# Kernel tuning notes

Measured on AMD Instinct MI355X. Metric: run time of the kernel, lower is better.

Reference implementation:

```python
import jax, jax.numpy as jnp
import numpy as np

N_QUBITS = 8          # == hidden_dim
DIM = 2 ** N_QUBITS   # statevector size
EMBED = 512
VOCAB = 50257
SEQ = 128
BATCH = 256


def _cnot_chain_perm(n):
    # CNOT(w,w+1) for w in 0..n-2, then CNOT(n-1,0); wire 0 = MSB.
    f = np.arange(2 ** n)
    pairs = [(w, w + 1) for w in range(n - 1)] + [(n - 1, 0)]
    for c, t in pairs:
        cbit = (f >> (n - 1 - c)) & 1
        f = f ^ (cbit << (n - 1 - t))
    inv = np.empty_like(f)
    inv[f] = np.arange(2 ** n)
    return inv

_PERM_INV = jnp.asarray(_cnot_chain_perm(N_QUBITS))
# signs[j, k] = <j|Z_k|j> = 1 - 2*bit_k(j), wire 0 = MSB
_j = np.arange(DIM)[:, None]
_SIGNS = jnp.asarray(1.0 - 2.0 * ((_j >> (N_QUBITS - 1 - np.arange(N_QUBITS))) & 1), dtype=jnp.float32)


def qlayer(y, theta):
    """RX(y_i) encoder + trainable RX(theta_i) (same axis -> RX(y+theta)),
    CNOT ring, PauliZ expectation per wire.  y: (B, n) -> (B, n)."""
    half = 0.5 * (y + theta)
    c = jnp.cos(half).astype(jnp.complex64)
    s = (-1j) * jnp.sin(half).astype(jnp.complex64)
    B = y.shape[0]
    state = jnp.ones((B, 1), jnp.complex64)
    for w in range(N_QUBITS):  # fixed small structural loop (kron build)
        amp = jnp.stack([c[:, w], s[:, w]], axis=1)  # (B, 2)
        state = (state[:, :, None] * amp[:, None, :]).reshape(B, -1)
    state = state[:, _PERM_INV]                       # apply CNOT ring
    probs = jnp.real(state * jnp.conj(state))         # (B, 2^n)
    return probs @ _SIGNS                             # (B, n)


def setup_inputs() -> dict:
    key = jax.random.key(0)
    ks = jax.random.split(key, 16)
    d_in = EMBED + N_QUBITS
    inp = {
        "sentence": jax.random.randint(ks[0], (SEQ, BATCH), 0, VOCAB),
        "features": jax.random.normal(ks[1], (BATCH, N_QUBITS), jnp.float32),
        "emb_table": 0.02 * jax.random.normal(ks[2], (VOCAB, EMBED), jnp.float32),
        "W_f": 0.05 * jax.random.normal(ks[3], (N_QUBITS, d_in), jnp.float32),
        "b_f": jnp.zeros((N_QUBITS,), jnp.float32),
        "W_i": 0.05 * jax.random.normal(ks[4], (N_QUBITS, d_in), jnp.float32),
        "b_i": jnp.zeros((N_QUBITS,), jnp.float32),
        "W_u": 0.05 * jax.random.normal(ks[5], (N_QUBITS, d_in), jnp.float32),
        "b_u": jnp.zeros((N_QUBITS,), jnp.float32),
        "W_o": 0.05 * jax.random.normal(ks[6], (N_QUBITS, d_in), jnp.float32),
        "b_o": jnp.zeros((N_QUBITS,), jnp.float32),
        "th_f": jax.random.normal(ks[7], (N_QUBITS,), jnp.float32),
        "th_i": jax.random.normal(ks[8], (N_QUBITS,), jnp.float32),
        "th_u": jax.random.normal(ks[9], (N_QUBITS,), jnp.float32),
        "th_o": jax.random.normal(ks[10], (N_QUBITS,), jnp.float32),
    }
    return inp


def reference(sentence, features, emb_table, W_f, b_f, W_i, b_i, W_u, b_u,
              W_o, b_o, th_f, th_i, th_u, th_o):
    embeds = emb_table[sentence]               # (T, B, E)
    B = embeds.shape[1]
    h0 = jnp.zeros((B, N_QUBITS), jnp.float32)
    c0 = jnp.zeros((B, N_QUBITS), jnp.float32)

    def step(carry, xt):
        hx, cx = carry
        comb = jnp.concatenate([xt, hx], axis=1)          # (B, E+H)
        f = jax.nn.sigmoid(qlayer(comb @ W_f.T + b_f, th_f))
        i = jax.nn.sigmoid(qlayer(comb @ W_i.T + b_i, th_i))
        g = jnp.tanh(qlayer(comb @ W_u.T + b_u, th_u))
        o = jax.nn.sigmoid(qlayer(comb @ W_o.T + b_o, th_o))
        cx = f * cx + i * g
        hx = o * jnp.tanh(cx)
        return (hx, cx), hx

    (hx, cx), outs = jax.lax.scan(step, (h0, c0), embeds)
    cls_input = outs[-1]                        # lstm_out[-1]: (B, H)
    return cls_input
```

## Files before the change

### kernel.cpp

```cpp
#include <hip/hip_runtime.h>
#include <hip/hip_bf16.h>

#define NQ     8
#define SEQL   128
#define BATCHN 256
#define EMBED  512
#define DIN    520
#define GSTR   32
#define GBSTR  40
#define INV2PI 0.15915494309189535f
#define WROW   524

typedef __attribute__((ext_vector_type(8))) short  bf16x8;
typedef __attribute__((ext_vector_type(4))) float  f32x4;
typedef unsigned int uint2v __attribute__((ext_vector_type(2)));

__device__ __forceinline__ bf16x8 cvt8(float4 u, float4 v) {
    union { unsigned w[4]; bf16x8 v8; } r;
    asm("v_cvt_pk_bf16_f32 %0, %1, %2" : "=v"(r.w[0]) : "v"(u.x), "v"(u.y));
    asm("v_cvt_pk_bf16_f32 %0, %1, %2" : "=v"(r.w[1]) : "v"(u.z), "v"(u.w));
    asm("v_cvt_pk_bf16_f32 %0, %1, %2" : "=v"(r.w[2]) : "v"(v.x), "v"(v.y));
    asm("v_cvt_pk_bf16_f32 %0, %1, %2" : "=v"(r.w[3]) : "v"(v.z), "v"(v.w));
    return r.v8;
}

#define DPP_QP(a,b,c,d) ((a)|((b)<<2)|((c)<<4)|((d)<<6))
#define DPP_SHL(n) (0x100+(n))
#define DPP_SHR(n) (0x110+(n))
#define DPP_ROR(n) (0x120+(n))

template<int CTRL>
__device__ __forceinline__ float updpf(float old_, float src) {
    return __int_as_float(__builtin_amdgcn_update_dpp(
        __float_as_int(old_), __float_as_int(src), CTRL, 0xF, 0xF, false));
}

__device__ __forceinline__ float xor16f(float x) {
    unsigned xu = (unsigned)__float_as_int(x);
    uint2v r = __builtin_amdgcn_permlane16_swap(xu, xu, false, false);
    return __int_as_float((int)(r.x ^ r.y ^ xu));
}

__device__ __forceinline__ float frcp(float x) { return __builtin_amdgcn_rcpf(x); }
__device__ __forceinline__ float fexp2(float x) { return __builtin_amdgcn_exp2f(x); }

#define LOG2E  1.4426950408889634f
#define LOG2E2 2.8853900817779268f

#define QSTEP(GV) do {                                                        \
    float sA = fmaf(H[0],Whp[0],fmaf(H[1],Whp[1],fmaf(H[2],Whp[2],H[3]*Whp[3]))); \
    float sB = fmaf(H[4],Whp[4],fmaf(H[5],Whp[5],fmaf(H[6],Whp[6],H[7]*Whp[7]))); \
    float cs = __builtin_amdgcn_cosf((GV) + sA + sB);                         \
    float p = cs, s;                                                          \
    s = updpf<DPP_SHR(1)>(1.0f, p); p *= (m1 ? s : 1.0f);                     \
    s = updpf<DPP_SHR(2)>(1.0f, p); p *= (m2 ? s : 1.0f);                     \
    s = updpf<DPP_SHR(4)>(1.0f, p); p *= (m4 ? s : 1.0f);                     \
    float v = jz ? 1.0f : cs;                                                 \
    v *= updpf<DPP_QP(1,0,3,2)>(v, v);                                        \
    v *= updpf<DPP_QP(2,3,0,1)>(v, v);                                        \
    float xl = updpf<DPP_SHL(4)>(v, v);                                       \
    float xr = updpf<DPP_SHR(4)>(v, v);                                       \
    v *= (m4 ? xr : xl);                                                      \
    float qv = jz ? v : p;                                                    \
    float act = fmaf(sk, frcp(1.0f + fexp2(ek * qv)), ok);                    \
    float A_  = act;                                                          \
    float B8  = updpf<DPP_ROR(8)>(A_, A_);                                    \
    float C16 = xor16f(A_);                                                   \
    float D24 = updpf<DPP_ROR(8)>(C16, C16);                                  \
    float fv = (g==0) ? A_ : (g==1) ? B8 : (g==2) ? C16 : D24;                \
    float iv = (g==1) ? A_ : (g==0) ? B8 : (g==3) ? C16 : D24;                \
    float uv = (g==2) ? A_ : (g==3) ? B8 : (g==0) ? C16 : D24;                \
    float ov = (g==3) ? A_ : (g==2) ? B8 : (g==1) ? C16 : D24;                \
    c_own = fmaf(fv, c_own, iv * uv);                                         \
    float tc = fmaf(-2.0f, frcp(1.0f + fexp2(LOG2E2 * c_own)), 1.0f);         \
    h_own = ov * tc;                                                          \
    H[0] = h_own;                                                             \
    H[1] = updpf<DPP_QP(1,0,3,2)>(H[0], H[0]);                                \
    H[2] = updpf<DPP_QP(2,3,0,1)>(H[0], H[0]);                                \
    H[3] = updpf<DPP_QP(2,3,0,1)>(H[1], H[1]);                                \
    _Pragma("unroll")                                                         \
    for (int rr = 0; rr < 4; ++rr) {                                          \
        float yl = updpf<DPP_SHL(4)>(H[rr], H[rr]);                           \
        float yr = updpf<DPP_SHR(4)>(H[rr], H[rr]);                           \
        H[4 + rr] = m4 ? yr : yl;                                             \
    }                                                                         \
} while (0)

#define MFMA_PHASE() do {                                                     \
    f32x4 acc0 = {0.f,0.f,0.f,0.f};                                           \
    f32x4 acc1 = {0.f,0.f,0.f,0.f};                                           \
    _Pragma("unroll")                                                         \
    for (int kc = 0; kc < 16; ++kc) {                                         \
        bf16x8 a = cvt8(ua[kc], va[kc]);                                      \
        const int kl_ = kc * 32 + q * 8;                                      \
        bf16x8 b0 = *reinterpret_cast<const bf16x8*>(&Wlds[lm][kl_]);         \
        bf16x8 b1 = *reinterpret_cast<const bf16x8*>(&Wlds[16 + lm][kl_]);    \
        acc0 = __builtin_amdgcn_mfma_f32_16x16x32_bf16(a, b0, acc0, 0, 0, 0); \
        acc1 = __builtin_amdgcn_mfma_f32_16x16x32_bf16(a, b1, acc1, 0, 0, 0); \
    }                                                                         \
    __syncthreads();                                                          \
    _Pragma("unroll")                                                         \
    for (int r_ = 0; r_ < 4; ++r_) {                                          \
        gbuf[(4*q + r_) * GBSTR + lm]      = fmaf(acc0[r_], INV2PI, bc0);     \
        gbuf[(4*q + r_) * GBSTR + 16 + lm] = fmaf(acc1[r_], INV2PI, bc1);     \
    }                                                                         \
    __syncthreads();                                                          \
    _Pragma("unroll")                                                         \
    for (int s_ = 0; s_ < 16; ++s_) gv[s_] = gbuf[s_ * GBSTR + l32];          \
} while (0)

__global__ __launch_bounds__(64, 1)
void k_fused(const int* __restrict__ sent, const float* __restrict__ emb,
             const float* __restrict__ Wf, const float* __restrict__ Wi,
             const float* __restrict__ Wu, const float* __restrict__ Wo,
             const float* __restrict__ bf, const float* __restrict__ bi,
             const float* __restrict__ bu, const float* __restrict__ bo,
             const float* __restrict__ thf, const float* __restrict__ thi,
             const float* __restrict__ thu, const float* __restrict__ tho,
             float* __restrict__ out)
{
    __shared__ short Wlds[32][WROW];
    __shared__ float gbuf[16 * GBSTR];

    const int tid = threadIdx.x;
    const int b   = blockIdx.x;
    const int l32 = tid & 31;
    const int g   = l32 >> 3;
    const int j   = l32 & 7;
    const int lm  = tid & 15;
    const int q   = tid >> 4;

    {
        const int c = tid & 31, seg = tid >> 5;
        const int gg = c >> 3, jj = c & 7;
        const float* W = (gg==0) ? Wf : (gg==1) ? Wi : (gg==2) ? Wu : Wo;
        const float* src = W + (size_t)jj * DIN + seg * 256;
        #pragma unroll
        for (int p = 0; p < 32; ++p) {
            float4 u = *reinterpret_cast<const float4*>(src + p * 8);
            float4 v = *reinterpret_cast<const float4*>(src + p * 8 + 4);
            *reinterpret_cast<bf16x8*>(&Wlds[c][seg * 256 + p * 8]) = cvt8(u, v);
        }
    }

    float bc0, bc1;
    {
        const int g0 = lm >> 3, j0 = lm & 7;
        const float* B0 = (g0==0) ? bf  : bi;
        const float* T0 = (g0==0) ? thf : thi;
        bc0 = (B0[j0] + T0[j0]) * INV2PI;
        const float* B1 = (g0==0) ? bu  : bo;
        const float* T1 = (g0==0) ? thu : tho;
        bc1 = (B1[j0] + T1[j0]) * INV2PI;
    }

    const float* Wsel = (g==0) ? Wf : (g==1) ? Wi : (g==2) ? Wu : Wo;
    float Whp[8];
    #pragma unroll
    for (int rr = 0; rr < 8; ++rr)
        Whp[rr] = Wsel[j * DIN + EMBED + (j ^ rr)] * INV2PI;

    __syncthreads();

    float4 ua[16], va[16];
    float  gv[16];
    {
        int tok0 = sent[lm * BATCHN + b];
        const float* ar = emb + (size_t)tok0 * EMBED;
        #pragma unroll
        for (int kc = 0; kc < 16; ++kc) {
            ua[kc] = *reinterpret_cast<const float4*>(ar + kc * 32 + q * 8);
            va[kc] = *reinterpret_cast<const float4*>(ar + kc * 32 + q * 8 + 4);
        }
    }
    int tokN = sent[(16 + lm) * BATCHN + b];
    MFMA_PHASE();

    float H[8];
    #pragma unroll
    for (int rr = 0; rr < 8; ++rr) H[rr] = 0.f;
    float c_own = 0.f, h_own = 0.f;

    const bool m1 = (j >= 1), m2 = (j >= 2), m4 = (j >= 4), jz = (j == 0);
    const bool isU = (g == 2);
    const float ek = isU ? LOG2E2 : -LOG2E;
    const float sk = isU ? -2.0f  : 1.0f;
    const float ok = isU ? 1.0f   : 0.0f;

    #pragma unroll 1
    for (int c = 0; c < 8; ++c) {
        int tokNN = 0;
        if (c < 6) tokNN = sent[((c + 2) * 16 + lm) * BATCHN + b];
        if (c < 7) {
            const float* an = emb + (size_t)tokN * EMBED;
            #pragma unroll
            for (int kc = 0; kc < 16; ++kc) {
                ua[kc] = *reinterpret_cast<const float4*>(an + kc * 32 + q * 8);
                va[kc] = *reinterpret_cast<const float4*>(an + kc * 32 + q * 8 + 4);
            }
        }
        asm volatile("" ::: "memory");

        #pragma unroll
        for (int s = 0; s < 16; ++s) QSTEP(gv[s]);

        if (c < 7) MFMA_PHASE();
        tokN = tokNN;
    }

    if (tid < 8) out[b * NQ + tid] = h_own;
}

extern "C" void kernel_launch(void* const* d_in, const int* in_sizes, int n_in,
                              void* d_out, int out_size, void* d_ws, size_t ws_size,
                              hipStream_t stream)
{
    const int*   sent = (const int*)  d_in[0];
    const float* emb  = (const float*)d_in[2];
    const float* Wf   = (const float*)d_in[3];
    const float* bf   = (const float*)d_in[4];
    const float* Wi   = (const float*)d_in[5];
    const float* bi   = (const float*)d_in[6];
    const float* Wu   = (const float*)d_in[7];
    const float* bu   = (const float*)d_in[8];
    const float* Wo   = (const float*)d_in[9];
    const float* bo   = (const float*)d_in[10];
    const float* thf  = (const float*)d_in[11];
    const float* thi  = (const float*)d_in[12];
    const float* thu  = (const float*)d_in[13];
    const float* tho  = (const float*)d_in[14];
    float* out = (float*)d_out;

    k_fused<<<BATCHN, 64, 0, stream>>>(sent, emb, Wf, Wi, Wu, Wo,
                                       bf, bi, bu, bo,
                                       thf, thi, thu, tho, out);
}
```

Baseline: 43.97 us.

## Split block into producer and consumer wavefronts with double-buffered gate input

The block grows to two wavefronts. One wave gathers embeddings and runs the MFMA input projection for the next 16-step chunk into one half of a double-buffered LDS gate buffer, while the other wave runs the serial quantum-LSTM recurrence on the current chunk. This overlaps the embedding gather and matrix phase with the recurrence instead of running them back to back in one wave. The cost is an extra wave per block, a block-wide barrier per chunk, and the producer's register footprint.

```diff
diff --git a/kernel.cpp b/kernel.cpp
--- a/kernel.cpp
+++ b/kernel.cpp
@@ -86,30 +86,34 @@
     }                                                                         \
 } while (0)
 
-#define MFMA_PHASE() do {                                                     \
+#define PRODUCE(DST, CH) do {                                                 \
+    int tok_ = sent[((CH) * 16 + lm) * BATCHN + b];                           \
+    const float* ar_ = emb + (size_t)tok_ * EMBED;                            \
+    float4 ua[16], va[16];                                                    \
+    _Pragma("unroll")                                                         \
+    for (int kc = 0; kc < 16; ++kc) {                                         \
+        ua[kc] = *reinterpret_cast<const float4*>(ar_ + kc * 32 + q * 8);     \
+        va[kc] = *reinterpret_cast<const float4*>(ar_ + kc * 32 + q * 8 + 4); \
+    }                                                                         \
     f32x4 acc0 = {0.f,0.f,0.f,0.f};                                           \
     f32x4 acc1 = {0.f,0.f,0.f,0.f};                                           \
     _Pragma("unroll")                                                         \
     for (int kc = 0; kc < 16; ++kc) {                                         \
-        bf16x8 a = cvt8(ua[kc], va[kc]);                                      \
+        bf16x8 a_ = cvt8(ua[kc], va[kc]);                                     \
         const int kl_ = kc * 32 + q * 8;                                      \
-        bf16x8 b0 = *reinterpret_cast<const bf16x8*>(&Wlds[lm][kl_]);         \
-        bf16x8 b1 = *reinterpret_cast<const bf16x8*>(&Wlds[16 + lm][kl_]);    \
-        acc0 = __builtin_amdgcn_mfma_f32_16x16x32_bf16(a, b0, acc0, 0, 0, 0); \
-        acc1 = __builtin_amdgcn_mfma_f32_16x16x32_bf16(a, b1, acc1, 0, 0, 0); \
-    }                                                                         \
-    __syncthreads();                                                          \
+        bf16x8 b0_ = *reinterpret_cast<const bf16x8*>(&Wlds[lm][kl_]);        \
+        bf16x8 b1_ = *reinterpret_cast<const bf16x8*>(&Wlds[16 + lm][kl_]);   \
+        acc0 = __builtin_amdgcn_mfma_f32_16x16x32_bf16(a_, b0_, acc0, 0,0,0); \
+        acc1 = __builtin_amdgcn_mfma_f32_16x16x32_bf16(a_, b1_, acc1, 0,0,0); \
+    }                                                                         \
     _Pragma("unroll")                                                         \
     for (int r_ = 0; r_ < 4; ++r_) {                                          \
-        gbuf[(4*q + r_) * GBSTR + lm]      = fmaf(acc0[r_], INV2PI, bc0);     \
-        gbuf[(4*q + r_) * GBSTR + 16 + lm] = fmaf(acc1[r_], INV2PI, bc1);     \
-    }                                                                         \
-    __syncthreads();                                                          \
-    _Pragma("unroll")                                                         \
-    for (int s_ = 0; s_ < 16; ++s_) gv[s_] = gbuf[s_ * GBSTR + l32];          \
+        (DST)[(4*q + r_) * GBSTR + lm]      = fmaf(acc0[r_], INV2PI, bc0);    \
+        (DST)[(4*q + r_) * GBSTR + 16 + lm] = fmaf(acc1[r_], INV2PI, bc1);    \
+    }                                                                         \
 } while (0)
 
-__global__ __launch_bounds__(64, 1)
+__global__ __launch_bounds__(128, 1)
 void k_fused(const int* __restrict__ sent, const float* __restrict__ emb,
              const float* __restrict__ Wf, const float* __restrict__ Wi,
              const float* __restrict__ Wu, const float* __restrict__ Wo,
@@ -120,31 +124,37 @@
              float* __restrict__ out)
 {
     __shared__ short Wlds[32][WROW];
-    __shared__ float gbuf[16 * GBSTR];
+    __shared__ float gbuf[2][16 * GBSTR];
 
     const int tid = threadIdx.x;
     const int b   = blockIdx.x;
+    const bool producer = (tid >= 64);
     const int l32 = tid & 31;
     const int g   = l32 >> 3;
     const int j   = l32 & 7;
     const int lm  = tid & 15;
-    const int q   = tid >> 4;
+    const int q   = (tid >> 4) & 3;
 
     {
         const int c = tid & 31, seg = tid >> 5;
         const int gg = c >> 3, jj = c & 7;
         const float* W = (gg==0) ? Wf : (gg==1) ? Wi : (gg==2) ? Wu : Wo;
-        const float* src = W + (size_t)jj * DIN + seg * 256;
+        const float* src = W + (size_t)jj * DIN + seg * 128;
         #pragma unroll
-        for (int p = 0; p < 32; ++p) {
+        for (int p = 0; p < 16; ++p) {
             float4 u = *reinterpret_cast<const float4*>(src + p * 8);
             float4 v = *reinterpret_cast<const float4*>(src + p * 8 + 4);
-            *reinterpret_cast<bf16x8*>(&Wlds[c][seg * 256 + p * 8]) = cvt8(u, v);
+            *reinterpret_cast<bf16x8*>(&Wlds[c][seg * 128 + p * 8]) = cvt8(u, v);
         }
     }
 
-    float bc0, bc1;
-    {
+    float Whp[8], H[8];
+    float c_own = 0.f, h_own = 0.f;
+    float bc0 = 0.f, bc1 = 0.f;
+    bool  m1 = false, m2 = false, m4 = false, jz = false;
+    float ek = 0.f, sk = 0.f, ok = 0.f;
+
+    if (producer) {
         const int g0 = lm >> 3, j0 = lm & 7;
         const float* B0 = (g0==0) ? bf  : bi;
         const float* T0 = (g0==0) ? thf : thi;
@@ -152,60 +162,39 @@
         const float* B1 = (g0==0) ? bu  : bo;
         const float* T1 = (g0==0) ? thu : tho;
         bc1 = (B1[j0] + T1[j0]) * INV2PI;
+    } else {
+        const float* Wsel = (g==0) ? Wf : (g==1) ? Wi : (g==2) ? Wu : Wo;
+        #pragma unroll
+        for (int rr = 0; rr < 8; ++rr) {
+            Whp[rr] = Wsel[j * DIN + EMBED + (j ^ rr)] * INV2PI;
+            H[rr]   = 0.f;
+        }
+        m1 = (j >= 1); m2 = (j >= 2); m4 = (j >= 4); jz = (j == 0);
+        const bool isU = (g == 2);
+        ek = isU ? LOG2E2 : -LOG2E;
+        sk = isU ? -2.0f  : 1.0f;
+        ok = isU ? 1.0f   : 0.0f;
     }
-
-    const float* Wsel = (g==0) ? Wf : (g==1) ? Wi : (g==2) ? Wu : Wo;
-    float Whp[8];
-    #pragma unroll
-    for (int rr = 0; rr < 8; ++rr)
-        Whp[rr] = Wsel[j * DIN + EMBED + (j ^ rr)] * INV2PI;
-
     __syncthreads();
 
-    float4 ua[16], va[16];
-    float  gv[16];
-    {
-        int tok0 = sent[lm * BATCHN + b];
-        const float* ar = emb + (size_t)tok0 * EMBED;
-        #pragma unroll
-        for (int kc = 0; kc < 16; ++kc) {
-            ua[kc] = *reinterpret_cast<const float4*>(ar + kc * 32 + q * 8);
-            va[kc] = *reinterpret_cast<const float4*>(ar + kc * 32 + q * 8 + 4);
-        }
-    }
-    int tokN = sent[(16 + lm) * BATCHN + b];
-    MFMA_PHASE();
-
-    float H[8];
-    #pragma unroll
-    for (int rr = 0; rr < 8; ++rr) H[rr] = 0.f;
-    float c_own = 0.f, h_own = 0.f;
-
-    const bool m1 = (j >= 1), m2 = (j >= 2), m4 = (j >= 4), jz = (j == 0);
-    const bool isU = (g == 2);
-    const float ek = isU ? LOG2E2 : -LOG2E;
-    const float sk = isU ? -2.0f  : 1.0f;
-    const float ok = isU ? 1.0f   : 0.0f;
+    if (producer) PRODUCE(&gbuf[0][0], 0);
+    __syncthreads();
 
     #pragma unroll 1
     for (int c = 0; c < 8; ++c) {
-        int tokNN = 0;
-        if (c < 6) tokNN = sent[((c + 2) * 16 + lm) * BATCHN + b];
-        if (c < 7) {
-            const float* an = emb + (size_t)tokN * EMBED;
+        if (producer) {
+            if (c < 7) PRODUCE(&gbuf[(c + 1) & 1][0], c + 1);
+        } else {
+            const float* gc = &gbuf[c & 1][l32];
+            float n0 = gc[0];
             #pragma unroll
-            for (int kc = 0; kc < 16; ++kc) {
-                ua[kc] = *reinterpret_cast<const float4*>(an + kc * 32 + q * 8);
-                va[kc] = *reinterpret_cast<const float4*>(an + kc * 32 + q * 8 + 4);
+            for (int s = 0; s < 16; ++s) {
+                float nn = (s < 15) ? gc[(s + 1) * GBSTR] : 0.f;
+                QSTEP(n0);
+                n0 = nn;
             }
         }
-        asm volatile("" ::: "memory");
-
-        #pragma unroll
-        for (int s = 0; s < 16; ++s) QSTEP(gv[s]);
-
-        if (c < 7) MFMA_PHASE();
-        tokN = tokNN;
+        __syncthreads();
     }
 
     if (tid < 8) out[b * NQ + tid] = h_own;
@@ -231,7 +220,7 @@
     const float* tho  = (const float*)d_in[14];
     float* out = (float*)d_out;
 
-    k_fused<<<BATCHN, 64, 0, stream>>>(sent, emb, Wf, Wi, Wu, Wo,
-                                       bf, bi, bu, bo,
-                                       thf, thi, thu, tho, out);
-}
+    k_fused<<<BATCHN, 128, 0, stream>>>(sent, emb, Wf, Wi, Wu, Wo,
+                                        bf, bi, bu, bo,
+                                        thf, thi, thu, tho, out);
+}
```

Result: faster. 35.92 us (median of 2 runs) (-18.3%).
